# Performance work log

Hardware: AMD Instinct MI355X
Metric: run time of the kernel (lower is better)

Reference implementation:

```python
import jax, jax.numpy as jnp
import numpy as np

NEG = -1e30  # log-space 'zero' that stays finite in fp32
EPS = 1e-7   # keras backend epsilon used by ctc_batch_cost


def _lse3(a, b, c):
    m = jnp.maximum(jnp.maximum(a, b), c)
    return m + jnp.log(jnp.exp(a - m) + jnp.exp(b - m) + jnp.exp(c - m))


def setup_inputs() -> dict:
    key = jax.random.key(0)
    k1, k2 = jax.random.split(key)
    B, T, C, U = 256, 1024, 128, 128
    logits = jax.random.normal(k1, (B, T, C), dtype=jnp.float32)
    y_pred = jax.nn.softmax(logits, axis=-1)  # ctc_batch_cost expects probabilities
    y_true = jax.random.randint(k2, (B, U), 0, C - 1)  # labels in [0, C-2]; blank = C-1
    return {"y_true": y_true, "y_pred": y_pred}


def reference(y_true, y_pred):
    # Faithful to tf.keras.backend.ctc_batch_cost with input_length = T,
    # label_length = U for every row; blank index = num_classes - 1.
    B, T, C = y_pred.shape
    U = y_true.shape[1]
    S = 2 * U + 1
    blank = C - 1

    logp = jnp.log(y_pred + EPS)  # [B, T, C]

    # Extended label sequence: blank, l1, blank, l2, ..., lU, blank
    ext = jnp.full((B, S), blank, dtype=y_true.dtype).at[:, 1::2].set(y_true)

    # Per-timestep log-probs of extended labels: [B, T, S]
    lp_ext = jnp.take_along_axis(logp, jnp.broadcast_to(ext[:, None, :], (B, T, S)), axis=2)

    # Skip transition s-2 -> s allowed iff ext[s] != blank and ext[s] != ext[s-2]
    allow = jnp.concatenate(
        [jnp.zeros((B, 2), bool), (ext[:, 2:] != blank) & (ext[:, 2:] != ext[:, :-2])],
        axis=1,
    )  # [B, S]

    alpha0 = (
        jnp.full((B, S), NEG, dtype=logp.dtype)
        .at[:, 0].set(lp_ext[:, 0, 0])
        .at[:, 1].set(lp_ext[:, 0, 1])
    )

    lp_t = jnp.moveaxis(lp_ext, 1, 0)  # [T, B, S]

    def step(alpha, lp):
        a1 = jnp.concatenate([jnp.full((B, 1), NEG, alpha.dtype), alpha[:, :-1]], axis=1)
        a2 = jnp.concatenate([jnp.full((B, 2), NEG, alpha.dtype), alpha[:, :-2]], axis=1)
        a2 = jnp.where(allow, a2, NEG)
        alpha = _lse3(alpha, a1, a2) + lp
        return alpha, None

    alphaT, _ = jax.lax.scan(step, alpha0, lp_t[1:])

    a, b = alphaT[:, S - 1], alphaT[:, S - 2]
    m = jnp.maximum(a, b)
    ll = m + jnp.log(jnp.exp(a - m) + jnp.exp(b - m))
    return (-ll)[:, None]  # [B, 1], matching ctc_batch_cost
```

## Files before the change

kernel.cpp:

```cpp
#include <hip/hip_runtime.h>
#include <math.h>


#define T_DIM 1024
#define C_DIM 128
#define U_DIM 128
#define LN2F  0.6931471805599453f

#define EPS_LIT "0x33d6bf95"

#define CMT(BP,BB) \
  "v_add_f32 v120, v124, " BB "\n\t" \
  "v_mov_b32 v121, v120\n\t" \
  "v_pk_add_f32 v[122:123], " BP ", v[124:125]\n\t"

#define ALPHA \
  "v_mov_b32_dpp v118, v115 wave_shr:1 row_mask:0xf bank_mask:0xf bound_ctrl:0\n\t" \
  "v_mov_b32 v119, v114\n\t" \
  "v_pk_add_f32 v[126:127], v[114:115], v[112:113]\n\t" \
  "v_pk_fma_f32 v[126:127], v[118:119], v[30:31], v[126:127]\n\t" \
  "v_pk_add_f32 v[112:113], v[112:113], v[118:119]\n\t" \
  "v_add_f32 v117, v115, v116\n\t" \
  "v_pk_mul_f32 v[114:115], v[126:127], v[122:123]\n\t" \
  "v_pk_mul_f32 v[112:113], v[112:113], v[120:121]\n\t" \
  "v_mul_f32 v116, v117, v120\n\t"

#define RENORM \
  "v_max_f32 v127, v112, v113\n\t" \
  "v_max_f32 v127, v127, v114\n\t" \
  "v_max_f32 v127, v127, v115\n\t" \
  "v_max_f32 v127, v127, v116\n\t" \
  "s_nop 1\n\t" \
  "v_max_f32_dpp v127, v127, v127 row_ror:8 row_mask:0xf bank_mask:0xf\n\t" \
  "s_nop 1\n\t" \
  "v_max_f32_dpp v127, v127, v127 row_ror:4 row_mask:0xf bank_mask:0xf\n\t" \
  "s_nop 1\n\t" \
  "v_max_f32_dpp v127, v127, v127 row_ror:2 row_mask:0xf bank_mask:0xf\n\t" \
  "s_nop 1\n\t" \
  "v_max_f32_dpp v127, v127, v127 row_ror:1 row_mask:0xf bank_mask:0xf\n\t" \
  "s_nop 1\n\t" \
  "v_readlane_b32 s91, v127, 0\n\t" \
  "v_readlane_b32 s92, v127, 16\n\t" \
  "v_readlane_b32 s93, v127, 32\n\t" \
  "v_readlane_b32 s94, v127, 48\n\t" \
  "s_nop 1\n\t" \
  "s_max_u32 s91, s91, s92\n\t" \
  "s_max_u32 s93, s93, s94\n\t" \
  "s_max_u32 s91, s91, s93\n\t" \
  "s_lshr_b32 s92, s91, 23\n\t" \
  "s_and_b32 s92, s92, 0xff\n\t" \
  "s_sub_u32 s93, 0x126, s92\n\t" \
  "s_min_u32 s93, s93, 0xfe\n\t" \
  "s_lshl_b32 s94, s93, 23\n\t" \
  "s_sub_u32 s95, 0x7f, s93\n\t" \
  "s_add_u32 %[EA], %[EA], s95\n\t" \
  "v_mul_f32 v112, s94, v112\n\t" \
  "v_mul_f32 v113, s94, v113\n\t" \
  "v_mul_f32 v114, s94, v114\n\t" \
  "v_mul_f32 v115, s94, v115\n\t" \
  "v_mul_f32 v116, s94, v116\n\t"

#define ST(...) ST_X(__VA_ARGS__)
#define ST_X(B0,B1,B2,BP,ROFF,RBOFF) \
  "s_waitcnt lgkmcnt(9)\n\t" \
  CMT(BP,B2) \
  "ds_read_b32 " B0 ", v12 offset:" ROFF "\n\t" \
  "ds_read_b32 " B1 ", v13 offset:" ROFF "\n\t" \
  "ds_read_b32 " B2 ", v14 offset:" RBOFF "\n\t" \
  ALPHA

#define K0 "v96","v97","v98","v[96:97]"
#define K1 "v100","v101","v102","v[100:101]"
#define K2 "v104","v105","v106","v[104:105]"
#define K3 "v108","v109","v110","v[108:109]"

#define PF2(SL) \
  "global_load_dwordx4 v[" SL "], v10, %[P]\n\t" \
  "v_add_u32 v10, 0x800, v10\n\t"
#define PWL2(SL,OFF) \
  "s_waitcnt vmcnt(15)\n\t" \
  "ds_write_b128 v11, v[" SL "] offset:" OFF "\n\t" \
  "global_load_dwordx4 v[" SL "], v10, %[P]\n\t" \
  "v_add_u32 v10, 0x800, v10\n\t"
#define PW2(VC,SL,OFF) \
  "s_waitcnt vmcnt(" VC ")\n\t" \
  "ds_write_b128 v11, v[" SL "] offset:" OFF "\n\t"
#define PBAR \
  "s_waitcnt lgkmcnt(0)\n\t" \
  "s_barrier\n\t"

__global__ __launch_bounds__(192) void ctc_alpha_kernel(
    const int*   __restrict__ y_true,
    const float* __restrict__ y_pred,
    float*       __restrict__ out,
    int B)
{
  __shared__ float4 ldsbuf[1024];

  const int b = blockIdx.x;
  if (b >= B) return;
  const int tid  = threadIdx.x;
  const int lane = tid & 63;
  const int wid  = tid >> 6;
  const unsigned lds_off = (unsigned)(uintptr_t)(void*)ldsbuf;

  if (wid >= 1) {
    const float* __restrict__ p = y_pred + (size_t)b * (T_DIM * C_DIM);
    const int boff   = (wid == 2) ? 1024 : 0;
    const int gvoff  = lane * 16 + boff;
    const int wraddr = (int)lds_off + lane * 16 + boff;
    asm volatile(
      "s_mov_b32 m0, -1\n\t"
      "v_mov_b32 v10, %[GV]\n\t"
      "v_mov_b32 v11, %[WA]\n\t"
      PF2("32:35") PF2("36:39") PF2("40:43") PF2("44:47")
      PF2("48:51") PF2("52:55") PF2("56:59") PF2("60:63")
      PF2("64:67") PF2("68:71") PF2("72:75") PF2("76:79")
      PF2("80:83") PF2("84:87") PF2("88:91") PF2("92:95")
      PWL2("32:35","0")    PWL2("36:39","2048")
      PWL2("40:43","4096") PWL2("44:47","6144")
      PBAR
      "s_mov_b32 s90, 14\n"
      "LP_%=:\n\t"
      PBAR PWL2("48:51","8192")  PWL2("52:55","10240")
      PBAR PWL2("56:59","12288") PWL2("60:63","14336")
      PBAR PWL2("64:67","0")     PWL2("68:71","2048")
      PBAR PWL2("72:75","4096")  PWL2("76:79","6144")
      PBAR PWL2("80:83","8192")  PWL2("84:87","10240")
      PBAR PWL2("88:91","12288") PWL2("92:95","14336")
      PBAR PWL2("32:35","0")     PWL2("36:39","2048")
      PBAR PWL2("40:43","4096")  PWL2("44:47","6144")
      "s_sub_u32 s90, s90, 1\n\t"
      "s_cmp_lg_u32 s90, 0\n\t"
      "s_cbranch_scc1 LP_%=\n\t"
      PBAR PWL2("48:51","8192")  PWL2("52:55","10240")
      PBAR PWL2("56:59","12288") PWL2("60:63","14336")
      PBAR PWL2("64:67","0")     PWL2("68:71","2048")
      PBAR PWL2("72:75","4096")  PWL2("76:79","6144")
      PBAR PWL2("80:83","8192")  PWL2("84:87","10240")
      PBAR PWL2("88:91","12288") PWL2("92:95","14336")
      PBAR PW2("15","32:35","0")     PW2("14","36:39","2048")
      PBAR PW2("13","40:43","4096")  PW2("12","44:47","6144")
      PBAR PW2("11","48:51","8192")  PW2("10","52:55","10240")
      PBAR PW2("9","56:59","12288")  PW2("8","60:63","14336")
      PBAR PW2("7","64:67","0")      PW2("6","68:71","2048")
      PBAR PW2("5","72:75","4096")   PW2("4","76:79","6144")
      PBAR PW2("3","80:83","8192")   PW2("2","84:87","10240")
      PBAR PW2("1","88:91","12288")  PW2("0","92:95","14336")
      PBAR
      PBAR
      :
      : [P]"s"(p), [GV]"v"(gvoff), [WA]"v"(wraddr)
      : "v10","v11",
        "v32","v33","v34","v35","v36","v37","v38","v39","v40","v41","v42","v43",
        "v44","v45","v46","v47","v48","v49","v50","v51","v52","v53","v54","v55",
        "v56","v57","v58","v59","v60","v61","v62","v63","v64","v65","v66","v67",
        "v68","v69","v70","v71","v72","v73","v74","v75","v76","v77","v78","v79",
        "v80","v81","v82","v83","v84","v85","v86","v87","v88","v89","v90","v91",
        "v92","v93","v94","v95",
        "s90","scc","memory");
    return;
  }

  const int* __restrict__ yb = y_true + b * U_DIM;
  const int blank = C_DIM - 1;
  const int ylab0 = yb[2 * lane];
  const int ylab1 = yb[2 * lane + 1];
  int yprev = blank;
  if (lane > 0) yprev = yb[2 * lane - 1];
  const float allow1 = (lane > 0 && ylab0 != blank && ylab0 != yprev) ? 1.0f : 0.0f;
  const float allow3 = (ylab1 != blank && ylab1 != ylab0)             ? 1.0f : 0.0f;

  const int rd1 = (int)lds_off + ylab0 * 4;
  const int rd3 = (int)lds_off + ylab1 * 4;
  const int rdb = (int)lds_off;

  const float init0 = (lane == 0) ? 1.0f : 0.0f;
  float a3out, a4out;
  int   e_acc = 0;

  asm volatile(
    "s_mov_b32 m0, -1\n\t"
    "v_mov_b32 v12, %[R1]\n\t"
    "v_mov_b32 v13, %[R3]\n\t"
    "v_mov_b32 v14, %[RB]\n\t"
    "v_mov_b32 v30, %[L1]\n\t"
    "v_mov_b32 v31, %[L3]\n\t"
    "v_mov_b32 v112, %[I0]\n\t"
    "v_mov_b32 v113, 0\n\t"
    "v_mov_b32 v114, 0\n\t"
    "v_mov_b32 v115, 0\n\t"
    "v_mov_b32 v116, 0\n\t"
    "v_mov_b32 v124, " EPS_LIT "\n\t"
    "v_mov_b32 v125, " EPS_LIT "\n\t"
    "s_barrier\n\t"
    "ds_read_b32 v96, v12 offset:0\n\t"
    "ds_read_b32 v97, v13 offset:0\n\t"
    "ds_read_b32 v98, v14 offset:508\n\t"
    "ds_read_b32 v100, v12 offset:512\n\t"
    "ds_read_b32 v101, v13 offset:512\n\t"
    "ds_read_b32 v102, v14 offset:1020\n\t"
    "ds_read_b32 v104, v12 offset:1024\n\t"
    "ds_read_b32 v105, v13 offset:1024\n\t"
    "ds_read_b32 v106, v14 offset:1532\n\t"
    "ds_read_b32 v108, v12 offset:1536\n\t"
    "ds_read_b32 v109, v13 offset:1536\n\t"
    "ds_read_b32 v110, v14 offset:2044\n\t"
    "s_mov_b32 s90, 32\n"
    "LM_%=:\n\t"
    "s_barrier\n\t"
    ST(K0,"2048","2556")   ST(K1,"2560","3068")   ST(K2,"3072","3580")   ST(K3,"3584","4092")
    ST(K0,"4096","4604")   ST(K1,"4608","5116")   ST(K2,"5120","5628")   ST(K3,"5632","6140")
    RENORM
    "s_barrier\n\t"
    ST(K0,"6144","6652")   ST(K1,"6656","7164")   ST(K2,"7168","7676")   ST(K3,"7680","8188")
    ST(K0,"8192","8700")   ST(K1,"8704","9212")   ST(K2,"9216","9724")   ST(K3,"9728","10236")
    RENORM
    "s_barrier\n\t"
    ST(K0,"10240","10748") ST(K1,"10752","11260") ST(K2,"11264","11772") ST(K3,"11776","12284")
    ST(K0,"12288","12796") ST(K1,"12800","13308") ST(K2,"13312","13820") ST(K3,"13824","14332")
    RENORM
    "s_barrier\n\t"
    ST(K0,"14336","14844") ST(K1,"14848","15356") ST(K2,"15360","15868") ST(K3,"15872","16380")
    ST(K0,"0","508")       ST(K1,"512","1020")    ST(K2,"1024","1532")   ST(K3,"1536","2044")
    RENORM
    "s_sub_u32 s90, s90, 1\n\t"
    "s_cmp_lg_u32 s90, 0\n\t"
    "s_cbranch_scc1 LM_%=\n\t"
    "s_waitcnt lgkmcnt(0)\n\t"
    "v_mov_b32 %[O3], v115\n\t"
    "v_mov_b32 %[O4], v116\n\t"
    : [O3]"=v"(a3out), [O4]"=v"(a4out), [EA]"+s"(e_acc)
    : [R1]"v"(rd1), [R3]"v"(rd3), [RB]"v"(rdb),
      [L1]"v"(allow1), [L3]"v"(allow3), [I0]"v"(init0)
    : "v12","v13","v14","v30","v31",
      "v96","v97","v98","v100","v101","v102",
      "v104","v105","v106","v108","v109","v110",
      "v112","v113","v114","v115","v116","v117","v118","v119","v120","v121",
      "v122","v123","v124","v125","v126","v127",
      "s90","s91","s92","s93","s94","s95","scc","memory");

  if (lane == 63) {
    float s = a3out + a4out;
    s = fmaxf(s, 1e-37f);
    float ll = logf(s) + (float)e_acc * LN2F;
    out[b] = -ll;
  }
}

extern "C" void kernel_launch(void* const* d_in, const int* in_sizes, int n_in,
                              void* d_out, int out_size, void* d_ws, size_t ws_size,
                              hipStream_t stream) {
  const int*   y_true = (const int*)d_in[0];
  const float* y_pred = (const float*)d_in[1];
  float*       out    = (float*)d_out;
  const int B = in_sizes[0] / U_DIM;
  ctc_alpha_kernel<<<dim3(B), dim3(192), 0, stream>>>(y_true, y_pred, out, B);
}
```

Measured before the change: 195.9 us.

## Move epsilon add to loader waves and read blank prob twice

The loader waves now add EPS to the probabilities before writing them to LDS. This takes the per-step epsilon adds (CMT) off the serial alpha recurrence wave. The compute wave reads the blank probability into two registers so it can use a packed multiply without a mov. It also splits the alpha update so the LDS wait comes after the head arithmetic, overlapping LDS latency with compute. In exchange it issues an extra ds_read per step and adds work to the loader waves.

```diff
diff --git a/kernel.cpp b/kernel.cpp
--- a/kernel.cpp
+++ b/kernel.cpp
@@ -9,21 +9,18 @@
 
 #define EPS_LIT "0x33d6bf95"
 
-#define CMT(BP,BB) \
-  "v_add_f32 v120, v124, " BB "\n\t" \
-  "v_mov_b32 v121, v120\n\t" \
-  "v_pk_add_f32 v[122:123], " BP ", v[124:125]\n\t"
-
-#define ALPHA \
+#define ALPHA_HEAD \
   "v_mov_b32_dpp v118, v115 wave_shr:1 row_mask:0xf bank_mask:0xf bound_ctrl:0\n\t" \
   "v_mov_b32 v119, v114\n\t" \
   "v_pk_add_f32 v[126:127], v[114:115], v[112:113]\n\t" \
   "v_pk_fma_f32 v[126:127], v[118:119], v[30:31], v[126:127]\n\t" \
   "v_pk_add_f32 v[112:113], v[112:113], v[118:119]\n\t" \
-  "v_add_f32 v117, v115, v116\n\t" \
-  "v_pk_mul_f32 v[114:115], v[126:127], v[122:123]\n\t" \
-  "v_pk_mul_f32 v[112:113], v[112:113], v[120:121]\n\t" \
-  "v_mul_f32 v116, v117, v120\n\t"
+  "v_add_f32 v117, v115, v116\n\t"
+
+#define ALPHA_TAIL(BP,CBP,CB0) \
+  "v_pk_mul_f32 v[114:115], v[126:127], " BP "\n\t" \
+  "v_pk_mul_f32 v[112:113], v[112:113], " CBP "\n\t" \
+  "v_mul_f32 v116, v117, " CB0 "\n\t"
 
 #define RENORM \
   "v_max_f32 v127, v112, v113\n\t" \
@@ -61,29 +58,34 @@
   "v_mul_f32 v116, s94, v116\n\t"
 
 #define ST(...) ST_X(__VA_ARGS__)
-#define ST_X(B0,B1,B2,BP,ROFF,RBOFF) \
-  "s_waitcnt lgkmcnt(9)\n\t" \
-  CMT(BP,B2) \
+#define ST_X(B0,B1,B2,B3,BP,CBP,CB0,ROFF,RBOFF) \
+  ALPHA_HEAD \
+  "s_waitcnt lgkmcnt(11)\n\t" \
+  ALPHA_TAIL(BP,CBP,CB0) \
   "ds_read_b32 " B0 ", v12 offset:" ROFF "\n\t" \
   "ds_read_b32 " B1 ", v13 offset:" ROFF "\n\t" \
   "ds_read_b32 " B2 ", v14 offset:" RBOFF "\n\t" \
-  ALPHA
-
-#define K0 "v96","v97","v98","v[96:97]"
-#define K1 "v100","v101","v102","v[100:101]"
-#define K2 "v104","v105","v106","v[104:105]"
-#define K3 "v108","v109","v110","v[108:109]"
+  "ds_read_b32 " B3 ", v14 offset:" RBOFF "\n\t"
+
+#define K0 "v96","v97","v98","v99","v[96:97]","v[98:99]","v98"
+#define K1 "v100","v101","v102","v103","v[100:101]","v[102:103]","v102"
+#define K2 "v104","v105","v106","v107","v[104:105]","v[106:107]","v106"
+#define K3 "v108","v109","v110","v111","v[108:109]","v[110:111]","v110"
 
 #define PF2(SL) \
   "global_load_dwordx4 v[" SL "], v10, %[P]\n\t" \
   "v_add_u32 v10, 0x800, v10\n\t"
-#define PWL2(SL,OFF) \
+#define PWL2(PA,PB,SL,OFF) \
   "s_waitcnt vmcnt(15)\n\t" \
+  "v_pk_add_f32 v[" PA "], v[" PA "], v[24:25]\n\t" \
+  "v_pk_add_f32 v[" PB "], v[" PB "], v[24:25]\n\t" \
   "ds_write_b128 v11, v[" SL "] offset:" OFF "\n\t" \
   "global_load_dwordx4 v[" SL "], v10, %[P]\n\t" \
   "v_add_u32 v10, 0x800, v10\n\t"
-#define PW2(VC,SL,OFF) \
+#define PW2(VC,PA,PB,SL,OFF) \
   "s_waitcnt vmcnt(" VC ")\n\t" \
+  "v_pk_add_f32 v[" PA "], v[" PA "], v[24:25]\n\t" \
+  "v_pk_add_f32 v[" PB "], v[" PB "], v[24:25]\n\t" \
   "ds_write_b128 v11, v[" SL "] offset:" OFF "\n\t"
 #define PBAR \
   "s_waitcnt lgkmcnt(0)\n\t" \
@@ -113,45 +115,47 @@
       "s_mov_b32 m0, -1\n\t"
       "v_mov_b32 v10, %[GV]\n\t"
       "v_mov_b32 v11, %[WA]\n\t"
+      "v_mov_b32 v24, " EPS_LIT "\n\t"
+      "v_mov_b32 v25, " EPS_LIT "\n\t"
       PF2("32:35") PF2("36:39") PF2("40:43") PF2("44:47")
       PF2("48:51") PF2("52:55") PF2("56:59") PF2("60:63")
       PF2("64:67") PF2("68:71") PF2("72:75") PF2("76:79")
       PF2("80:83") PF2("84:87") PF2("88:91") PF2("92:95")
-      PWL2("32:35","0")    PWL2("36:39","2048")
-      PWL2("40:43","4096") PWL2("44:47","6144")
+      PWL2("32:33","34:35","32:35","0")    PWL2("36:37","38:39","36:39","2048")
+      PWL2("40:41","42:43","40:43","4096") PWL2("44:45","46:47","44:47","6144")
       PBAR
       "s_mov_b32 s90, 14\n"
       "LP_%=:\n\t"
-      PBAR PWL2("48:51","8192")  PWL2("52:55","10240")
-      PBAR PWL2("56:59","12288") PWL2("60:63","14336")
-      PBAR PWL2("64:67","0")     PWL2("68:71","2048")
-      PBAR PWL2("72:75","4096")  PWL2("76:79","6144")
-      PBAR PWL2("80:83","8192")  PWL2("84:87","10240")
-      PBAR PWL2("88:91","12288") PWL2("92:95","14336")
-      PBAR PWL2("32:35","0")     PWL2("36:39","2048")
-      PBAR PWL2("40:43","4096")  PWL2("44:47","6144")
+      PBAR PWL2("48:49","50:51","48:51","8192")   PWL2("52:53","54:55","52:55","10240")
+      PBAR PWL2("56:57","58:59","56:59","12288")  PWL2("60:61","62:63","60:63","14336")
+      PBAR PWL2("64:65","66:67","64:67","0")      PWL2("68:69","70:71","68:71","2048")
+      PBAR PWL2("72:73","74:75","72:75","4096")   PWL2("76:77","78:79","76:79","6144")
+      PBAR PWL2("80:81","82:83","80:83","8192")   PWL2("84:85","86:87","84:87","10240")
+      PBAR PWL2("88:89","90:91","88:91","12288")  PWL2("92:93","94:95","92:95","14336")
+      PBAR PWL2("32:33","34:35","32:35","0")      PWL2("36:37","38:39","36:39","2048")
+      PBAR PWL2("40:41","42:43","40:43","4096")   PWL2("44:45","46:47","44:47","6144")
       "s_sub_u32 s90, s90, 1\n\t"
       "s_cmp_lg_u32 s90, 0\n\t"
       "s_cbranch_scc1 LP_%=\n\t"
-      PBAR PWL2("48:51","8192")  PWL2("52:55","10240")
-      PBAR PWL2("56:59","12288") PWL2("60:63","14336")
-      PBAR PWL2("64:67","0")     PWL2("68:71","2048")
-      PBAR PWL2("72:75","4096")  PWL2("76:79","6144")
-      PBAR PWL2("80:83","8192")  PWL2("84:87","10240")
-      PBAR PWL2("88:91","12288") PWL2("92:95","14336")
-      PBAR PW2("15","32:35","0")     PW2("14","36:39","2048")
-      PBAR PW2("13","40:43","4096")  PW2("12","44:47","6144")
-      PBAR PW2("11","48:51","8192")  PW2("10","52:55","10240")
-      PBAR PW2("9","56:59","12288")  PW2("8","60:63","14336")
-      PBAR PW2("7","64:67","0")      PW2("6","68:71","2048")
-      PBAR PW2("5","72:75","4096")   PW2("4","76:79","6144")
-      PBAR PW2("3","80:83","8192")   PW2("2","84:87","10240")
-      PBAR PW2("1","88:91","12288")  PW2("0","92:95","14336")
+      PBAR PWL2("48:49","50:51","48:51","8192")   PWL2("52:53","54:55","52:55","10240")
+      PBAR PWL2("56:57","58:59","56:59","12288")  PWL2("60:61","62:63","60:63","14336")
+      PBAR PWL2("64:65","66:67","64:67","0")      PWL2("68:69","70:71","68:71","2048")
+      PBAR PWL2("72:73","74:75","72:75","4096")   PWL2("76:77","78:79","76:79","6144")
+      PBAR PWL2("80:81","82:83","80:83","8192")   PWL2("84:85","86:87","84:87","10240")
+      PBAR PWL2("88:89","90:91","88:91","12288")  PWL2("92:93","94:95","92:95","14336")
+      PBAR PW2("15","32:33","34:35","32:35","0")    PW2("14","36:37","38:39","36:39","2048")
+      PBAR PW2("13","40:41","42:43","40:43","4096") PW2("12","44:45","46:47","44:47","6144")
+      PBAR PW2("11","48:49","50:51","48:51","8192") PW2("10","52:53","54:55","52:55","10240")
+      PBAR PW2("9","56:57","58:59","56:59","12288") PW2("8","60:61","62:63","60:63","14336")
+      PBAR PW2("7","64:65","66:67","64:67","0")     PW2("6","68:69","70:71","68:71","2048")
+      PBAR PW2("5","72:73","74:75","72:75","4096")  PW2("4","76:77","78:79","76:79","6144")
+      PBAR PW2("3","80:81","82:83","80:83","8192")  PW2("2","84:85","86:87","84:87","10240")
+      PBAR PW2("1","88:89","90:91","88:91","12288") PW2("0","92:93","94:95","92:95","14336")
       PBAR
       PBAR
       :
       : [P]"s"(p), [GV]"v"(gvoff), [WA]"v"(wraddr)
-      : "v10","v11",
+      : "v10","v11","v24","v25",
         "v32","v33","v34","v35","v36","v37","v38","v39","v40","v41","v42","v43",
         "v44","v45","v46","v47","v48","v49","v50","v51","v52","v53","v54","v55",
         "v56","v57","v58","v59","v60","v61","v62","v63","v64","v65","v66","v67",
@@ -191,21 +195,23 @@
     "v_mov_b32 v114, 0\n\t"
     "v_mov_b32 v115, 0\n\t"
     "v_mov_b32 v116, 0\n\t"
-    "v_mov_b32 v124, " EPS_LIT "\n\t"
-    "v_mov_b32 v125, " EPS_LIT "\n\t"
     "s_barrier\n\t"
     "ds_read_b32 v96, v12 offset:0\n\t"
     "ds_read_b32 v97, v13 offset:0\n\t"
     "ds_read_b32 v98, v14 offset:508\n\t"
+    "ds_read_b32 v99, v14 offset:508\n\t"
     "ds_read_b32 v100, v12 offset:512\n\t"
     "ds_read_b32 v101, v13 offset:512\n\t"
     "ds_read_b32 v102, v14 offset:1020\n\t"
+    "ds_read_b32 v103, v14 offset:1020\n\t"
     "ds_read_b32 v104, v12 offset:1024\n\t"
     "ds_read_b32 v105, v13 offset:1024\n\t"
     "ds_read_b32 v106, v14 offset:1532\n\t"
+    "ds_read_b32 v107, v14 offset:1532\n\t"
     "ds_read_b32 v108, v12 offset:1536\n\t"
     "ds_read_b32 v109, v13 offset:1536\n\t"
     "ds_read_b32 v110, v14 offset:2044\n\t"
+    "ds_read_b32 v111, v14 offset:2044\n\t"
     "s_mov_b32 s90, 32\n"
     "LM_%=:\n\t"
     "s_barrier\n\t"
@@ -234,10 +240,10 @@
     : [R1]"v"(rd1), [R3]"v"(rd3), [RB]"v"(rdb),
       [L1]"v"(allow1), [L3]"v"(allow3), [I0]"v"(init0)
     : "v12","v13","v14","v30","v31",
-      "v96","v97","v98","v100","v101","v102",
-      "v104","v105","v106","v108","v109","v110",
-      "v112","v113","v114","v115","v116","v117","v118","v119","v120","v121",
-      "v122","v123","v124","v125","v126","v127",
+      "v96","v97","v98","v99","v100","v101","v102","v103",
+      "v104","v105","v106","v107","v108","v109","v110","v111",
+      "v112","v113","v114","v115","v116","v117","v118","v119",
+      "v126","v127",
       "s90","s91","s92","s93","s94","s95","scc","memory");
 
   if (lane == 63) {
```

Result: no change. 196.4 us (+0.2%).
